# Kernel tuning notes

Measured on AMD Instinct MI355X. Metric: run time of the kernel, lower is better.

Reference implementation:

```python
import itertools
import jax, jax.numpy as jnp
import numpy as np

ACTION_BLADES = (0, 5, 6, 7, 8, 9, 10, 15)  # even subalgebra of Cl(3,0,1)
INPUT_BLADES = (11, 12, 13)                  # trivector point coords e012,e013,e023
E123_IDX = 14                                # homogeneous coordinate blade


def _build_cayley():
    """Cayley table M[i,j,k]: e_i * e_j = sum_k M[i,j,k] e_k for metric [0,1,1,1]."""
    metric = [0, 1, 1, 1]
    blades = [()]
    for g in range(1, 5):
        blades += list(itertools.combinations(range(4), g))
    idx = {b: i for i, b in enumerate(blades)}
    M = np.zeros((16, 16, 16), np.float32)
    for i, a in enumerate(blades):
        for j, b in enumerate(blades):
            arr = list(a) + list(b)
            sign = 1
            n = len(arr)
            for p in range(n):            # bubble sort, counting swaps
                for q in range(n - 1):
                    if arr[q] > arr[q + 1]:
                        arr[q], arr[q + 1] = arr[q + 1], arr[q]
                        sign = -sign
            res, k = [], 0
            while k < len(arr):           # contract repeated generators with metric
                if k + 1 < len(arr) and arr[k] == arr[k + 1]:
                    sign *= metric[arr[k]]
                    k += 2
                else:
                    res.append(arr[k])
                    k += 1
            if sign != 0:
                M[i, j, idx[tuple(res)]] += sign
    grades = np.array([len(b) for b in blades])
    rev = ((-1.0) ** (grades * (grades - 1) // 2)).astype(np.float32)  # reverse signs
    return M, rev


CAYLEY_NP, REVERSE_NP = _build_cayley()


def setup_inputs() -> dict:
    key = jax.random.key(0)
    k1, k2, k3, k4 = jax.random.split(key, 4)
    B, I, O = 4096, 512, 512
    x = jax.random.normal(k1, (B, I, 3), jnp.float32)
    weight = jax.random.normal(k2, (O, I), jnp.float32) * (1.0 / np.sqrt(I))
    action = jax.random.normal(k3, (O, I, 8), jnp.float32) * 0.1
    embed_e0 = jax.random.normal(k4, (I, 1), jnp.float32)
    return {"x": x, "weight": weight, "action": action, "embed_e0": embed_e0}


def reference(x, weight, action, embed_e0):
    M = jnp.asarray(CAYLEY_NP)
    rev = jnp.asarray(REVERSE_NP)
    o, i, _ = action.shape
    b = x.shape[0]
    ab = jnp.array(ACTION_BLADES)
    ib = jnp.array(INPUT_BLADES)
    # embed action into full 16-blade multivector; k_ = reverse(k)
    k = jnp.zeros((o, i, 16), x.dtype).at[..., ab].set(action)
    k_ = k * rev
    # embed input points as trivectors, set e123 component from embed_e0
    xf = jnp.zeros((b, i, 16), x.dtype).at[..., ib].set(x)
    xf = xf.at[..., E123_IDX].set(jnp.broadcast_to(embed_e0[:, 0], (b, i)))
    # left/right geometric-product kernels (unflattened)
    k_l = jnp.einsum('ijk,pqi->jpkq', M, k)    # (16, o, 16, i)
    k_r = jnp.einsum('ijk,pqk->jpiq', M, k_)   # (16, o, 16, i)
    # sandwich conjugation + channel mixing, fused einsum
    out = jnp.einsum('oi,poqi,qori,bir->bop', weight, k_r, k_l, xf)
    return out[..., ib]


if __name__ == "__main__":
    out = reference(**setup_inputs())
    print(out.shape)
```

## Files before the change

### kernel.cpp

```cpp
#include <hip/hip_runtime.h>
#include <hip/hip_bf16.h>


#define B_DIM 4096
#define I_DIM 512
#define O_DIM 512
#define N_DIM (O_DIM * 3)
#define K_DIM (I_DIM * 3)

typedef __attribute__((ext_vector_type(8))) short bf16x8;
typedef __attribute__((ext_vector_type(4))) float f32x4;

__device__ __forceinline__ unsigned short f2bf(float f) {
    unsigned u = __float_as_uint(f);
    unsigned r = (u + 0x7fffu + ((u >> 16) & 1u)) >> 16;
    return (unsigned short)r;
}

__device__ __forceinline__ void gload_lds16(const void* g, void* l) {
    __builtin_amdgcn_global_load_lds(
        (const __attribute__((address_space(1))) unsigned*)g,
        (__attribute__((address_space(3))) unsigned*)l, 16, 0, 0);
}

struct Cayley {
    float M[16][16][16];
    float rev[16];
    constexpr Cayley() : M{}, rev{} {
        const unsigned masks[16] = {0u, 1u, 2u, 4u, 8u, 3u, 5u, 9u, 6u, 10u,
                                    12u, 7u, 11u, 13u, 14u, 15u};
        int idx_of[16] = {};
        for (int i = 0; i < 16; ++i) idx_of[masks[i]] = i;
        const int metric[4] = {0, 1, 1, 1};
        for (int i = 0; i < 16; ++i) {
            unsigned a = masks[i];
            for (int j = 0; j < 16; ++j) {
                unsigned b = masks[j];
                int swaps = 0;
                for (int jb = 0; jb < 4; ++jb)
                    if ((b >> jb) & 1u)
                        for (int ia = jb + 1; ia < 4; ++ia)
                            if ((a >> ia) & 1u) ++swaps;
                int sign = (swaps & 1) ? -1 : 1;
                unsigned common = a & b;
                for (int g = 0; g < 4; ++g)
                    if ((common >> g) & 1u) sign *= metric[g];
                if (sign != 0) M[i][j][idx_of[a ^ b]] += (float)sign;
            }
            int grade = 0;
            for (int g = 0; g < 4; ++g) grade += (int)((a >> g) & 1u);
            rev[i] = ((grade * (grade - 1) / 2) % 2) ? -1.f : 1.f;
        }
    }
};
constexpr Cayley CAY{};

__global__ __launch_bounds__(256) void build_w(const float* __restrict__ weight,
                                               const float* __restrict__ action,
                                               const float* __restrict__ e0,
                                               unsigned short* __restrict__ Bw,
                                               float* __restrict__ bias) {
    const int t = blockIdx.x * 256 + threadIdx.x;
    const int o = t >> 9;
    const int i = t & 511;
    const int lane = threadIdx.x & 63;

    float a[8];
    const float* ap = action + (size_t)t * 8;
#pragma unroll
    for (int j = 0; j < 8; ++j) a[j] = ap[j];

    float kv[16], kr[16];
#pragma unroll
    for (int j = 0; j < 16; ++j) { kv[j] = 0.f; kr[j] = 0.f; }
    constexpr int AB[8] = {0, 5, 6, 7, 8, 9, 10, 15};
#pragma unroll
    for (int j = 0; j < 8; ++j) {
        kv[AB[j]] = a[j];
        kr[AB[j]] = a[j] * CAY.rev[AB[j]];
    }

    constexpr int PB[3] = {11, 12, 13};
    constexpr int RB[4] = {11, 12, 13, 14};

    float Am[3][16];
#pragma unroll
    for (int pp = 0; pp < 3; ++pp)
#pragma unroll
        for (int q = 0; q < 16; ++q) {
            float s = 0.f;
#pragma unroll
            for (int tt = 0; tt < 16; ++tt) s += CAY.M[q][PB[pp]][tt] * kr[tt];
            Am[pp][q] = s;
        }

    float Bm[16][4];
#pragma unroll
    for (int q = 0; q < 16; ++q)
#pragma unroll
        for (int rr = 0; rr < 4; ++rr) {
            float s = 0.f;
#pragma unroll
            for (int m = 0; m < 16; ++m) s += CAY.M[m][q][RB[rr]] * kv[m];
            Bm[q][rr] = s;
        }

    const float w = weight[t];
    const float e0i = e0[i];
#pragma unroll
    for (int pp = 0; pp < 3; ++pp) {
        float r0 = 0.f, r1 = 0.f, r2 = 0.f, r3 = 0.f;
#pragma unroll
        for (int q = 0; q < 16; ++q) {
            r0 += Am[pp][q] * Bm[q][0];
            r1 += Am[pp][q] * Bm[q][1];
            r2 += Am[pp][q] * Bm[q][2];
            r3 += Am[pp][q] * Bm[q][3];
        }
        unsigned short* bp = Bw + (size_t)(o * 3 + pp) * K_DIM + i * 3;
        bp[0] = f2bf(w * r0);
        bp[1] = f2bf(w * r1);
        bp[2] = f2bf(w * r2);
        float s = w * r3 * e0i;
#pragma unroll
        for (int off = 32; off; off >>= 1) s += __shfl_down(s, off, 64);
        if (lane == 0) atomicAdd(bias + o * 3 + pp, s);
    }
}

__global__ __launch_bounds__(256) void pack_x(const float* __restrict__ x,
                                              unsigned short* __restrict__ A) {
    const size_t t = (size_t)blockIdx.x * 256 + threadIdx.x;
    const float4* xp = (const float4*)(x + t * 8);
    const float4 v0 = xp[0], v1 = xp[1];
    const float xs[8] = {v0.x, v0.y, v0.z, v0.w, v1.x, v1.y, v1.z, v1.w};
    unsigned short ov[8];
#pragma unroll
    for (int q = 0; q < 8; ++q) ov[q] = f2bf(xs[q]);
    *(uint4*)(A + t * 8) = *(const uint4*)ov;
}

__global__ __launch_bounds__(256) void gemm_bf16(const unsigned short* __restrict__ A,
                                                 const unsigned short* __restrict__ Bw,
                                                 const float* __restrict__ bias,
                                                 float* __restrict__ C) {
    __shared__ unsigned short As[64 * 64];
    __shared__ unsigned short Bs[128 * 64];

    const int tid = threadIdx.x;
    const int wave = tid >> 6, lane = tid & 63;

    const int bid = blockIdx.x;
    const int swz = (bid & 7) * 96 + (bid >> 3);
    const int mt = swz / 12, nt = swz - mt * 12;
    const int m0 = mt * 64, n0 = nt * 128;
    const int wr = wave >> 1, wc = wave & 1;

    const int sA0 = tid, sA1 = tid + 256;
    const unsigned short* aSrc0 =
        A + (size_t)(m0 + (sA0 >> 3)) * K_DIM + (((sA0 & 7) ^ ((sA0 >> 3) & 7)) * 8);
    const unsigned short* aSrc1 =
        A + (size_t)(m0 + (sA1 >> 3)) * K_DIM + (((sA1 & 7) ^ ((sA1 >> 3) & 7)) * 8);
    unsigned short* aDst0 = &As[(size_t)(0 * 256 + wave * 64) * 8];
    unsigned short* aDst1 = &As[(size_t)(1 * 256 + wave * 64) * 8];

    const unsigned short* bSrc[4];
    unsigned short* bDst[4];
#pragma unroll
    for (int q = 0; q < 4; ++q) {
        const int s = tid + q * 256;
        bSrc[q] = Bw + (size_t)(n0 + (s >> 3)) * K_DIM +
                  (((s & 7) ^ ((s >> 3) & 7)) * 8);
        bDst[q] = &Bs[(size_t)(q * 256 + wave * 64) * 8];
    }

    const int frow = lane & 15;
    const int g0 = lane >> 4;

    f32x4 acc[2][4] = {};

    for (int k0 = 0; k0 < K_DIM; k0 += 64) {
        gload_lds16(aSrc0 + k0, aDst0);
        gload_lds16(aSrc1 + k0, aDst1);
#pragma unroll
        for (int q = 0; q < 4; ++q) gload_lds16(bSrc[q] + k0, bDst[q]);
        __syncthreads();

        bf16x8 af[2][2], bf[2][4];
#pragma unroll
        for (int kh = 0; kh < 2; ++kh) {
#pragma unroll
            for (int mi = 0; mi < 2; ++mi) {
                const int r = wr * 32 + mi * 16 + frow;
                af[kh][mi] = *(const bf16x8*)&As[r * 64 + ((g0 + kh * 4) ^ (r & 7)) * 8];
            }
#pragma unroll
            for (int ni = 0; ni < 4; ++ni) {
                const int r = wc * 64 + ni * 16 + frow;
                bf[kh][ni] = *(const bf16x8*)&Bs[r * 64 + ((g0 + kh * 4) ^ (r & 7)) * 8];
            }
        }
#pragma unroll
        for (int kh = 0; kh < 2; ++kh)
#pragma unroll
            for (int mi = 0; mi < 2; ++mi)
#pragma unroll
                for (int ni = 0; ni < 4; ++ni)
                    acc[mi][ni] = __builtin_amdgcn_mfma_f32_16x16x32_bf16(
                        af[kh][mi], bf[kh][ni], acc[mi][ni], 0, 0, 0);
        __syncthreads();
    }

    const int crow = (lane >> 4) * 4;
    const int ccol = lane & 15;
#pragma unroll
    for (int mi = 0; mi < 2; ++mi)
#pragma unroll
        for (int ni = 0; ni < 4; ++ni) {
            const int n = n0 + wc * 64 + ni * 16 + ccol;
            const float bv = bias[n];
            float* cp = C + (size_t)(m0 + wr * 32 + mi * 16 + crow) * N_DIM + n;
#pragma unroll
            for (int j = 0; j < 4; ++j) cp[(size_t)j * N_DIM] = acc[mi][ni][j] + bv;
        }
}

extern "C" void kernel_launch(void* const* d_in, const int* in_sizes, int n_in,
                              void* d_out, int out_size, void* d_ws, size_t ws_size,
                              hipStream_t stream) {
    const float* x      = (const float*)d_in[0];
    const float* weight = (const float*)d_in[1];
    const float* action = (const float*)d_in[2];
    const float* e0     = (const float*)d_in[3];
    float* out = (float*)d_out;

    unsigned short* Bw = (unsigned short*)d_ws;
    unsigned short* Ap = Bw + (size_t)N_DIM * K_DIM;
    float* bias = (float*)(Ap + (size_t)B_DIM * K_DIM);

    hipMemsetAsync(bias, 0, N_DIM * sizeof(float), stream);
    hipLaunchKernelGGL(build_w, dim3((O_DIM * I_DIM) / 256), dim3(256), 0, stream,
                       weight, action, e0, Bw, bias);
    hipLaunchKernelGGL(pack_x, dim3((B_DIM * K_DIM / 8) / 256), dim3(256), 0, stream,
                       x, Ap);
    hipLaunchKernelGGL(gemm_bf16, dim3(768), dim3(256), 0, stream,
                       Ap, Bw, bias, out);
}
```

Before: 52.65 us.

## Double-buffer GEMM LDS tiles and split bias into atomic-free kernel

The GEMM main loop now uses two LDS buffers, so the global-to-LDS load of the next K tile is issued before the MFMA work on the current tile, with one barrier per tile instead of two. The bias computation moves out of build_w into a separate per-output kernel that reduces with shuffles and writes directly. This removes the memset and the atomics but adds a kernel launch. Double buffering doubles LDS per block (48KB), which may reduce occupancy.

```diff
diff --git a/kernel.cpp b/kernel.cpp
--- a/kernel.cpp
+++ b/kernel.cpp
@@ -7,6 +7,7 @@
 #define O_DIM 512
 #define N_DIM (O_DIM * 3)
 #define K_DIM (I_DIM * 3)
+#define NT (K_DIM / 64)
 
 typedef __attribute__((ext_vector_type(8))) short bf16x8;
 typedef __attribute__((ext_vector_type(4))) float f32x4;
@@ -57,13 +58,10 @@
 
 __global__ __launch_bounds__(256) void build_w(const float* __restrict__ weight,
                                                const float* __restrict__ action,
-                                               const float* __restrict__ e0,
-                                               unsigned short* __restrict__ Bw,
-                                               float* __restrict__ bias) {
+                                               unsigned short* __restrict__ Bw) {
     const int t = blockIdx.x * 256 + threadIdx.x;
     const int o = t >> 9;
     const int i = t & 511;
-    const int lane = threadIdx.x & 63;
 
     float a[8];
     const float* ap = action + (size_t)t * 8;
@@ -81,7 +79,7 @@
     }
 
     constexpr int PB[3] = {11, 12, 13};
-    constexpr int RB[4] = {11, 12, 13, 14};
+    constexpr int RB[3] = {11, 12, 13};
 
     float Am[3][16];
 #pragma unroll
@@ -94,11 +92,11 @@
             Am[pp][q] = s;
         }
 
-    float Bm[16][4];
+    float Bm[16][3];
 #pragma unroll
     for (int q = 0; q < 16; ++q)
 #pragma unroll
-        for (int rr = 0; rr < 4; ++rr) {
+        for (int rr = 0; rr < 3; ++rr) {
             float s = 0.f;
 #pragma unroll
             for (int m = 0; m < 16; ++m) s += CAY.M[m][q][RB[rr]] * kv[m];
@@ -106,25 +104,84 @@
         }
 
     const float w = weight[t];
-    const float e0i = e0[i];
 #pragma unroll
     for (int pp = 0; pp < 3; ++pp) {
-        float r0 = 0.f, r1 = 0.f, r2 = 0.f, r3 = 0.f;
+        float r0 = 0.f, r1 = 0.f, r2 = 0.f;
 #pragma unroll
         for (int q = 0; q < 16; ++q) {
             r0 += Am[pp][q] * Bm[q][0];
             r1 += Am[pp][q] * Bm[q][1];
             r2 += Am[pp][q] * Bm[q][2];
-            r3 += Am[pp][q] * Bm[q][3];
         }
         unsigned short* bp = Bw + (size_t)(o * 3 + pp) * K_DIM + i * 3;
         bp[0] = f2bf(w * r0);
         bp[1] = f2bf(w * r1);
         bp[2] = f2bf(w * r2);
-        float s = w * r3 * e0i;
-#pragma unroll
-        for (int off = 32; off; off >>= 1) s += __shfl_down(s, off, 64);
-        if (lane == 0) atomicAdd(bias + o * 3 + pp, s);
+    }
+}
+
+__global__ __launch_bounds__(64) void build_bias(const float* __restrict__ weight,
+                                                 const float* __restrict__ action,
+                                                 const float* __restrict__ e0,
+                                                 float* __restrict__ bias) {
+    const int o = blockIdx.x;
+    const int lane = threadIdx.x;
+    constexpr int AB[8] = {0, 5, 6, 7, 8, 9, 10, 15};
+    constexpr int PB[3] = {11, 12, 13};
+
+    float s0 = 0.f, s1 = 0.f, s2 = 0.f;
+#pragma unroll
+    for (int ii = 0; ii < 8; ++ii) {
+        const int i = lane + ii * 64;
+        const int t = o * I_DIM + i;
+        float a[8];
+        const float* ap = action + (size_t)t * 8;
+#pragma unroll
+        for (int j = 0; j < 8; ++j) a[j] = ap[j];
+        float kv[16], kr[16];
+#pragma unroll
+        for (int j = 0; j < 16; ++j) { kv[j] = 0.f; kr[j] = 0.f; }
+#pragma unroll
+        for (int j = 0; j < 8; ++j) {
+            kv[AB[j]] = a[j];
+            kr[AB[j]] = a[j] * CAY.rev[AB[j]];
+        }
+        float Bm3[16];
+#pragma unroll
+        for (int q = 0; q < 16; ++q) {
+            float s = 0.f;
+#pragma unroll
+            for (int m = 0; m < 16; ++m) s += CAY.M[m][q][14] * kv[m];
+            Bm3[q] = s;
+        }
+        float T3[3];
+#pragma unroll
+        for (int pp = 0; pp < 3; ++pp) {
+            float acc = 0.f;
+#pragma unroll
+            for (int q = 0; q < 16; ++q) {
+                float am = 0.f;
+#pragma unroll
+                for (int tt = 0; tt < 16; ++tt) am += CAY.M[q][PB[pp]][tt] * kr[tt];
+                acc += am * Bm3[q];
+            }
+            T3[pp] = acc;
+        }
+        const float we = weight[t] * e0[i];
+        s0 += we * T3[0];
+        s1 += we * T3[1];
+        s2 += we * T3[2];
+    }
+#pragma unroll
+    for (int off = 32; off; off >>= 1) {
+        s0 += __shfl_down(s0, off, 64);
+        s1 += __shfl_down(s1, off, 64);
+        s2 += __shfl_down(s2, off, 64);
+    }
+    if (lane == 0) {
+        bias[o * 3 + 0] = s0;
+        bias[o * 3 + 1] = s1;
+        bias[o * 3 + 2] = s2;
     }
 }
 
@@ -144,8 +201,8 @@
                                                  const unsigned short* __restrict__ Bw,
                                                  const float* __restrict__ bias,
                                                  float* __restrict__ C) {
-    __shared__ unsigned short As[64 * 64];
-    __shared__ unsigned short Bs[128 * 64];
+    __shared__ unsigned short As0[64 * 64], As1[64 * 64];
+    __shared__ unsigned short Bs0[128 * 64], Bs1[128 * 64];
 
     const int tid = threadIdx.x;
     const int wave = tid >> 6, lane = tid & 63;
@@ -161,17 +218,17 @@
         A + (size_t)(m0 + (sA0 >> 3)) * K_DIM + (((sA0 & 7) ^ ((sA0 >> 3) & 7)) * 8);
     const unsigned short* aSrc1 =
         A + (size_t)(m0 + (sA1 >> 3)) * K_DIM + (((sA1 & 7) ^ ((sA1 >> 3) & 7)) * 8);
-    unsigned short* aDst0 = &As[(size_t)(0 * 256 + wave * 64) * 8];
-    unsigned short* aDst1 = &As[(size_t)(1 * 256 + wave * 64) * 8];
+    const int aOff0 = (0 * 256 + wave * 64) * 8;
+    const int aOff1 = (1 * 256 + wave * 64) * 8;
 
     const unsigned short* bSrc[4];
-    unsigned short* bDst[4];
+    int bOff[4];
 #pragma unroll
     for (int q = 0; q < 4; ++q) {
         const int s = tid + q * 256;
         bSrc[q] = Bw + (size_t)(n0 + (s >> 3)) * K_DIM +
                   (((s & 7) ^ ((s >> 3) & 7)) * 8);
-        bDst[q] = &Bs[(size_t)(q * 256 + wave * 64) * 8];
+        bOff[q] = (q * 256 + wave * 64) * 8;
     }
 
     const int frow = lane & 15;
@@ -179,37 +236,61 @@
 
     f32x4 acc[2][4] = {};
 
-    for (int k0 = 0; k0 < K_DIM; k0 += 64) {
-        gload_lds16(aSrc0 + k0, aDst0);
-        gload_lds16(aSrc1 + k0, aDst1);
-#pragma unroll
-        for (int q = 0; q < 4; ++q) gload_lds16(bSrc[q] + k0, bDst[q]);
+#define STAGE(AS, BS, K0)                                   \
+    do {                                                    \
+        gload_lds16(aSrc0 + (K0), (AS) + aOff0);            \
+        gload_lds16(aSrc1 + (K0), (AS) + aOff1);            \
+        _Pragma("unroll")                                   \
+        for (int q = 0; q < 4; ++q)                         \
+            gload_lds16(bSrc[q] + (K0), (BS) + bOff[q]);    \
+    } while (0)
+
+#define COMPUTE(AS, BS)                                                        \
+    do {                                                                       \
+        bf16x8 af[2][2], bfr[2][4];                                            \
+        _Pragma("unroll")                                                      \
+        for (int kh = 0; kh < 2; ++kh) {                                       \
+            _Pragma("unroll")                                                  \
+            for (int mi = 0; mi < 2; ++mi) {                                   \
+                const int r = wr * 32 + mi * 16 + frow;                        \
+                af[kh][mi] =                                                   \
+                    *(const bf16x8*)&(AS)[r * 64 + ((g0 + kh * 4) ^ (r & 7)) * 8]; \
+            }                                                                  \
+            _Pragma("unroll")                                                  \
+            for (int ni = 0; ni < 4; ++ni) {                                   \
+                const int r = wc * 64 + ni * 16 + frow;                        \
+                bfr[kh][ni] =                                                  \
+                    *(const bf16x8*)&(BS)[r * 64 + ((g0 + kh * 4) ^ (r & 7)) * 8]; \
+            }                                                                  \
+        }                                                                      \
+        _Pragma("unroll")                                                      \
+        for (int kh = 0; kh < 2; ++kh)                                         \
+            _Pragma("unroll")                                                  \
+            for (int mi = 0; mi < 2; ++mi)                                     \
+                _Pragma("unroll")                                              \
+                for (int ni = 0; ni < 4; ++ni)                                 \
+                    acc[mi][ni] = __builtin_amdgcn_mfma_f32_16x16x32_bf16(     \
+                        af[kh][mi], bfr[kh][ni], acc[mi][ni], 0, 0, 0);        \
+    } while (0)
+
+    STAGE(As0, Bs0, 0);
+    __syncthreads();
+
+    for (int t = 0; t < NT - 2; t += 2) {
+        STAGE(As1, Bs1, (t + 1) * 64);
+        COMPUTE(As0, Bs0);
         __syncthreads();
-
-        bf16x8 af[2][2], bf[2][4];
-#pragma unroll
-        for (int kh = 0; kh < 2; ++kh) {
-#pragma unroll
-            for (int mi = 0; mi < 2; ++mi) {
-                const int r = wr * 32 + mi * 16 + frow;
-                af[kh][mi] = *(const bf16x8*)&As[r * 64 + ((g0 + kh * 4) ^ (r & 7)) * 8];
-            }
-#pragma unroll
-            for (int ni = 0; ni < 4; ++ni) {
-                const int r = wc * 64 + ni * 16 + frow;
-                bf[kh][ni] = *(const bf16x8*)&Bs[r * 64 + ((g0 + kh * 4) ^ (r & 7)) * 8];
-            }
-        }
-#pragma unroll
-        for (int kh = 0; kh < 2; ++kh)
-#pragma unroll
-            for (int mi = 0; mi < 2; ++mi)
-#pragma unroll
-                for (int ni = 0; ni < 4; ++ni)
-                    acc[mi][ni] = __builtin_amdgcn_mfma_f32_16x16x32_bf16(
-                        af[kh][mi], bf[kh][ni], acc[mi][ni], 0, 0, 0);
+        STAGE(As0, Bs0, (t + 2) * 64);
+        COMPUTE(As1, Bs1);
         __syncthreads();
     }
+    STAGE(As1, Bs1, (NT - 1) * 64);
+    COMPUTE(As0, Bs0);
+    __syncthreads();
+    COMPUTE(As1, Bs1);
+
+#undef STAGE
+#undef COMPUTE
 
     const int crow = (lane >> 4) * 4;
     const int ccol = lane & 15;
@@ -238,9 +319,10 @@
     unsigned short* Ap = Bw + (size_t)N_DIM * K_DIM;
     float* bias = (float*)(Ap + (size_t)B_DIM * K_DIM);
 
-    hipMemsetAsync(bias, 0, N_DIM * sizeof(float), stream);
     hipLaunchKernelGGL(build_w, dim3((O_DIM * I_DIM) / 256), dim3(256), 0, stream,
-                       weight, action, e0, Bw, bias);
+                       weight, action, Bw);
+    hipLaunchKernelGGL(build_bias, dim3(O_DIM), dim3(64), 0, stream,
+                       weight, action, e0, bias);
     hipLaunchKernelGGL(pack_x, dim3((B_DIM * K_DIM / 8) / 256), dim3(256), 0, stream,
                        x, Ap);
     hipLaunchKernelGGL(gemm_bf16, dim3(768), dim3(256), 0, stream,
```

Measured after the change: 51.00 us. -3.1%, faster.

## Fuse prep kernels, drop memset/atomics, triple-buffer GEMM with 128x96 tiles

Applied to the files above, without the earlier changes.

Merges pack_x and build_w into one prep launch. Bias is now reduced per block through shared memory, so the memset and atomics are gone. The GEMM moves to 512-thread blocks with 128x96 tiles and BK=32, and uses a three-stage LDS ring with async global_load_lds and explicit vmcnt waits so loads overlap MFMA work. The intent is to cut launch overhead and hide memory latency, at the cost of a new LDS layout and a changed tile shape. Correctness of the new LDS layout relies on the hand-tuned waitcnt counts.

```diff
diff --git a/kernel.cpp b/kernel.cpp
--- a/kernel.cpp
+++ b/kernel.cpp
@@ -7,6 +7,8 @@
 #define O_DIM 512
 #define N_DIM (O_DIM * 3)
 #define K_DIM (I_DIM * 3)
+#define BK 32
+#define NT (K_DIM / BK)
 
 typedef __attribute__((ext_vector_type(8))) short bf16x8;
 typedef __attribute__((ext_vector_type(4))) float f32x4;
@@ -55,15 +57,37 @@
 };
 constexpr Cayley CAY{};
 
-__global__ __launch_bounds__(256) void build_w(const float* __restrict__ weight,
-                                               const float* __restrict__ action,
-                                               const float* __restrict__ e0,
-                                               unsigned short* __restrict__ Bw,
-                                               float* __restrict__ bias) {
-    const int t = blockIdx.x * 256 + threadIdx.x;
-    const int o = t >> 9;
-    const int i = t & 511;
-    const int lane = threadIdx.x & 63;
+__global__ __launch_bounds__(512) void prep(const float* __restrict__ x,
+                                            const float* __restrict__ weight,
+                                            const float* __restrict__ action,
+                                            const float* __restrict__ e0,
+                                            unsigned short* __restrict__ A,
+                                            unsigned short* __restrict__ Bw,
+                                            float* __restrict__ bias) {
+    const int bid = blockIdx.x;
+    const int tid = threadIdx.x;
+
+    if (bid < 1536) {
+        const size_t t = (size_t)bid * 512 + tid;
+        const float4* xp = (const float4*)(x + t * 8);
+        const float4 v0 = xp[0], v1 = xp[1];
+        const float xs[8] = {v0.x, v0.y, v0.z, v0.w, v1.x, v1.y, v1.z, v1.w};
+        unsigned short ov[8];
+#pragma unroll
+        for (int q = 0; q < 8; ++q) ov[q] = f2bf(xs[q]);
+        *(uint4*)(A + t * 8) = *(const uint4*)ov;
+        return;
+    }
+
+    const int o = bid - 1536;
+    const int i = tid;
+    const int t = o * I_DIM + i;
+    const int wave = tid >> 6, lane = tid & 63;
+    __shared__ float red[8][3];
+
+    constexpr int AB[8] = {0, 5, 6, 7, 8, 9, 10, 15};
+    constexpr int PB[3] = {11, 12, 13};
+    constexpr int RB[4] = {11, 12, 13, 14};
 
     float a[8];
     const float* ap = action + (size_t)t * 8;
@@ -73,16 +97,12 @@
     float kv[16], kr[16];
 #pragma unroll
     for (int j = 0; j < 16; ++j) { kv[j] = 0.f; kr[j] = 0.f; }
-    constexpr int AB[8] = {0, 5, 6, 7, 8, 9, 10, 15};
 #pragma unroll
     for (int j = 0; j < 8; ++j) {
         kv[AB[j]] = a[j];
         kr[AB[j]] = a[j] * CAY.rev[AB[j]];
     }
 
-    constexpr int PB[3] = {11, 12, 13};
-    constexpr int RB[4] = {11, 12, 13, 14};
-
     float Am[3][16];
 #pragma unroll
     for (int pp = 0; pp < 3; ++pp)
@@ -107,6 +127,7 @@
 
     const float w = weight[t];
     const float e0i = e0[i];
+    float sb[3];
 #pragma unroll
     for (int pp = 0; pp < 3; ++pp) {
         float r0 = 0.f, r1 = 0.f, r2 = 0.f, r3 = 0.f;
@@ -121,103 +142,132 @@
         bp[0] = f2bf(w * r0);
         bp[1] = f2bf(w * r1);
         bp[2] = f2bf(w * r2);
-        float s = w * r3 * e0i;
-#pragma unroll
-        for (int off = 32; off; off >>= 1) s += __shfl_down(s, off, 64);
-        if (lane == 0) atomicAdd(bias + o * 3 + pp, s);
-    }
-}
-
-__global__ __launch_bounds__(256) void pack_x(const float* __restrict__ x,
-                                              unsigned short* __restrict__ A) {
-    const size_t t = (size_t)blockIdx.x * 256 + threadIdx.x;
-    const float4* xp = (const float4*)(x + t * 8);
-    const float4 v0 = xp[0], v1 = xp[1];
-    const float xs[8] = {v0.x, v0.y, v0.z, v0.w, v1.x, v1.y, v1.z, v1.w};
-    unsigned short ov[8];
-#pragma unroll
-    for (int q = 0; q < 8; ++q) ov[q] = f2bf(xs[q]);
-    *(uint4*)(A + t * 8) = *(const uint4*)ov;
-}
-
-__global__ __launch_bounds__(256) void gemm_bf16(const unsigned short* __restrict__ A,
-                                                 const unsigned short* __restrict__ Bw,
-                                                 const float* __restrict__ bias,
-                                                 float* __restrict__ C) {
-    __shared__ unsigned short As[64 * 64];
-    __shared__ unsigned short Bs[128 * 64];
+        sb[pp] = w * r3 * e0i;
+    }
+
+#pragma unroll
+    for (int off = 32; off; off >>= 1) {
+#pragma unroll
+        for (int pp = 0; pp < 3; ++pp) sb[pp] += __shfl_down(sb[pp], off, 64);
+    }
+    if (lane == 0) {
+#pragma unroll
+        for (int pp = 0; pp < 3; ++pp) red[wave][pp] = sb[pp];
+    }
+    __syncthreads();
+    if (tid == 0) {
+#pragma unroll
+        for (int pp = 0; pp < 3; ++pp) {
+            float s = 0.f;
+#pragma unroll
+            for (int wv = 0; wv < 8; ++wv) s += red[wv][pp];
+            bias[o * 3 + pp] = s;
+        }
+    }
+}
+
+__global__ __launch_bounds__(512, 4) void gemm_bf16(
+        const unsigned short* __restrict__ A,
+        const unsigned short* __restrict__ Bw,
+        const float* __restrict__ bias,
+        float* __restrict__ C) {
+    __shared__ unsigned short As0[4096], As1[4096], As2[4096];
+    __shared__ unsigned short Bs0[3072], Bs1[3072], Bs2[3072];
 
     const int tid = threadIdx.x;
     const int wave = tid >> 6, lane = tid & 63;
 
     const int bid = blockIdx.x;
-    const int swz = (bid & 7) * 96 + (bid >> 3);
-    const int mt = swz / 12, nt = swz - mt * 12;
-    const int m0 = mt * 64, n0 = nt * 128;
+    const int swz = (bid & 7) * 64 + (bid >> 3);
+    const int mt = swz >> 4, nt = swz & 15;
+    const int m0 = mt * 128, n0 = nt * 96;
     const int wr = wave >> 1, wc = wave & 1;
 
-    const int sA0 = tid, sA1 = tid + 256;
-    const unsigned short* aSrc0 =
-        A + (size_t)(m0 + (sA0 >> 3)) * K_DIM + (((sA0 & 7) ^ ((sA0 >> 3) & 7)) * 8);
-    const unsigned short* aSrc1 =
-        A + (size_t)(m0 + (sA1 >> 3)) * K_DIM + (((sA1 & 7) ^ ((sA1 >> 3) & 7)) * 8);
-    unsigned short* aDst0 = &As[(size_t)(0 * 256 + wave * 64) * 8];
-    unsigned short* aDst1 = &As[(size_t)(1 * 256 + wave * 64) * 8];
-
-    const unsigned short* bSrc[4];
-    unsigned short* bDst[4];
-#pragma unroll
-    for (int q = 0; q < 4; ++q) {
-        const int s = tid + q * 256;
-        bSrc[q] = Bw + (size_t)(n0 + (s >> 3)) * K_DIM +
-                  (((s & 7) ^ ((s >> 3) & 7)) * 8);
-        bDst[q] = &Bs[(size_t)(q * 256 + wave * 64) * 8];
-    }
+    const int arow = (tid >> 5) * 8 + (tid & 7);
+    const int acs = (tid >> 3) & 3;
+    const unsigned short* aSrc = A + (size_t)(m0 + arow) * K_DIM + acs * 8;
+    const int brow = (tid >> 5) * 8 + (tid & 7);
+    const int bcs = (tid >> 3) & 3;
+    const unsigned short* bSrc = Bw + (size_t)(n0 + brow) * K_DIM + bcs * 8;
+    const bool hasB = tid < 384;
 
     const int frow = lane & 15;
     const int g0 = lane >> 4;
-
-    f32x4 acc[2][4] = {};
-
-    for (int k0 = 0; k0 < K_DIM; k0 += 64) {
-        gload_lds16(aSrc0 + k0, aDst0);
-        gload_lds16(aSrc1 + k0, aDst1);
-#pragma unroll
-        for (int q = 0; q < 4; ++q) gload_lds16(bSrc[q] + k0, bDst[q]);
-        __syncthreads();
-
-        bf16x8 af[2][2], bf[2][4];
-#pragma unroll
-        for (int kh = 0; kh < 2; ++kh) {
-#pragma unroll
-            for (int mi = 0; mi < 2; ++mi) {
-                const int r = wr * 32 + mi * 16 + frow;
-                af[kh][mi] = *(const bf16x8*)&As[r * 64 + ((g0 + kh * 4) ^ (r & 7)) * 8];
-            }
-#pragma unroll
-            for (int ni = 0; ni < 4; ++ni) {
-                const int r = wc * 64 + ni * 16 + frow;
-                bf[kh][ni] = *(const bf16x8*)&Bs[r * 64 + ((g0 + kh * 4) ^ (r & 7)) * 8];
-            }
-        }
-#pragma unroll
-        for (int kh = 0; kh < 2; ++kh)
-#pragma unroll
-            for (int mi = 0; mi < 2; ++mi)
-#pragma unroll
-                for (int ni = 0; ni < 4; ++ni)
-                    acc[mi][ni] = __builtin_amdgcn_mfma_f32_16x16x32_bf16(
-                        af[kh][mi], bf[kh][ni], acc[mi][ni], 0, 0, 0);
-        __syncthreads();
-    }
+    int aro[2], bro[3];
+#pragma unroll
+    for (int mi = 0; mi < 2; ++mi) {
+        const int r = wr * 32 + mi * 16 + frow;
+        aro[mi] = ((r >> 3) * 32 + g0 * 8 + (r & 7)) * 8;
+    }
+#pragma unroll
+    for (int ni = 0; ni < 3; ++ni) {
+        const int r = wc * 48 + ni * 16 + frow;
+        bro[ni] = ((r >> 3) * 32 + g0 * 8 + (r & 7)) * 8;
+    }
+
+    f32x4 acc[2][3] = {};
+
+#define STAGE(AS, BS, T)                                     \
+    do {                                                     \
+        gload_lds16(aSrc + (T) * BK, (AS) + tid * 8);        \
+        if (hasB) gload_lds16(bSrc + (T) * BK, (BS) + tid * 8); \
+    } while (0)
+
+#define COMPUTE(AS, BS)                                                   \
+    do {                                                                  \
+        bf16x8 af[2], bfr[3];                                             \
+        _Pragma("unroll")                                                 \
+        for (int mi = 0; mi < 2; ++mi)                                    \
+            af[mi] = *(const bf16x8*)&(AS)[aro[mi]];                      \
+        _Pragma("unroll")                                                 \
+        for (int ni = 0; ni < 3; ++ni)                                    \
+            bfr[ni] = *(const bf16x8*)&(BS)[bro[ni]];                     \
+        _Pragma("unroll")                                                 \
+        for (int mi = 0; mi < 2; ++mi)                                    \
+            _Pragma("unroll")                                             \
+            for (int ni = 0; ni < 3; ++ni)                                \
+                acc[mi][ni] = __builtin_amdgcn_mfma_f32_16x16x32_bf16(    \
+                    af[mi], bfr[ni], acc[mi][ni], 0, 0, 0);               \
+    } while (0)
+
+#define WAITW                                                      \
+    do {                                                           \
+        if (hasB) asm volatile("s_waitcnt vmcnt(2)" ::: "memory"); \
+        else      asm volatile("s_waitcnt vmcnt(1)" ::: "memory"); \
+        __builtin_amdgcn_s_barrier();                              \
+    } while (0)
+#define WAIT0                                                \
+    do {                                                     \
+        asm volatile("s_waitcnt vmcnt(0)" ::: "memory");     \
+        __builtin_amdgcn_s_barrier();                        \
+    } while (0)
+
+    STAGE(As0, Bs0, 0);
+    STAGE(As1, Bs1, 1);
+
+#pragma unroll 1
+    for (int u = 0; u < 15; ++u) {
+        const int t = u * 3;
+        WAITW; COMPUTE(As0, Bs0); STAGE(As2, Bs2, t + 2);
+        WAITW; COMPUTE(As1, Bs1); STAGE(As0, Bs0, t + 3);
+        WAITW; COMPUTE(As2, Bs2); STAGE(As1, Bs1, t + 4);
+    }
+    WAITW; COMPUTE(As0, Bs0); STAGE(As2, Bs2, 47);
+    WAITW; COMPUTE(As1, Bs1);
+    WAIT0; COMPUTE(As2, Bs2);
+
+#undef STAGE
+#undef COMPUTE
+#undef WAITW
+#undef WAIT0
 
     const int crow = (lane >> 4) * 4;
     const int ccol = lane & 15;
 #pragma unroll
     for (int mi = 0; mi < 2; ++mi)
 #pragma unroll
-        for (int ni = 0; ni < 4; ++ni) {
-            const int n = n0 + wc * 64 + ni * 16 + ccol;
+        for (int ni = 0; ni < 3; ++ni) {
+            const int n = n0 + wc * 48 + ni * 16 + ccol;
             const float bv = bias[n];
             float* cp = C + (size_t)(m0 + wr * 32 + mi * 16 + crow) * N_DIM + n;
 #pragma unroll
@@ -238,11 +288,8 @@
     unsigned short* Ap = Bw + (size_t)N_DIM * K_DIM;
     float* bias = (float*)(Ap + (size_t)B_DIM * K_DIM);
 
-    hipMemsetAsync(bias, 0, N_DIM * sizeof(float), stream);
-    hipLaunchKernelGGL(build_w, dim3((O_DIM * I_DIM) / 256), dim3(256), 0, stream,
-                       weight, action, e0, Bw, bias);
-    hipLaunchKernelGGL(pack_x, dim3((B_DIM * K_DIM / 8) / 256), dim3(256), 0, stream,
-                       x, Ap);
-    hipLaunchKernelGGL(gemm_bf16, dim3(768), dim3(256), 0, stream,
+    hipLaunchKernelGGL(prep, dim3(2048), dim3(512), 0, stream,
+                       x, weight, action, e0, Ap, Bw, bias);
+    hipLaunchKernelGGL(gemm_bf16, dim3(512), dim3(512), 0, stream,
                        Ap, Bw, bias, out);
 }
```

After: 59.77 us. 13.5% more time.
